# Kernel optimization log

Measured on AMD Instinct MI355X. Metric: run time of the kernel, lower is better.

The kernel has to match this reference:

```python
import jax, jax.numpy as jnp
import numpy as np
from jax import lax

DT = 0.1

def setup_inputs() -> dict:
    key = jax.random.key(0)
    ks = jax.random.split(key, 6)
    T, B, D, H, O = 4096, 16, 256, 256, 256
    x = jax.random.normal(ks[0], (T, B, D), dtype=jnp.float32)
    U_w = jax.random.normal(ks[1], (H, D), dtype=jnp.float32) / np.sqrt(D)
    U_b = jax.random.normal(ks[2], (H,), dtype=jnp.float32) * 0.1
    # underlying parameter of the ExpLambda parametrization: weight = expm(W_log)
    W_log = jax.random.normal(ks[3], (H, H), dtype=jnp.float32) * 0.01
    c_w = jax.random.normal(ks[4], (O, H), dtype=jnp.float32) / np.sqrt(H)
    c_b = jax.random.normal(ks[5], (O,), dtype=jnp.float32) * 0.1
    return {"x": x, "U_w": U_w, "U_b": U_b, "W_log": W_log, "c_w": c_w, "c_b": c_b}

def reference(x, U_w, U_b, W_log, c_w, c_b):
    # x: [T, B, D] (time-major, matching torch.transpose(x,0,1) in the original)
    T, B, D = x.shape
    H = W_log.shape[0]
    Wexp = jax.scipy.linalg.expm(W_log)          # parametrized recurrent weight
    u = jnp.einsum('tbd,hd->tbh', x, U_w) + U_b  # precompute U(x) for all steps

    def step(h, u_t):
        # h_next = h + dt * tanh(u_t - W h)
        h_next = h + DT * jnp.tanh(u_t - h @ Wexp.T)
        return h_next, h_next

    h0 = jnp.zeros((B, H), dtype=x.dtype)
    h_final, hidden = lax.scan(step, h0, u)       # hidden: [T, B, H]
    out = jnp.einsum('tbh,oh->tbo', hidden, c_w) + c_b
    # original returns h_next.unsqueeze(1) on a (1,B,H) tensor -> (1,1,B,H)
    return out, h_final[None, None]
```

## Files before the change

kernel.cpp:

```cpp
#include <hip/hip_runtime.h>
#include <math.h>

#define T_STEPS 4096
#define NB 16
#define NH 256
#define BH (NB * NH)
#define DT_STEP 0.1f

typedef __attribute__((ext_vector_type(8))) short short8;
typedef __attribute__((ext_vector_type(4))) float f32x4;

__global__ __launch_bounds__(1024) void k_init_S(const float* __restrict__ A,
                                                 float* __restrict__ S) {
    int idx = blockIdx.x * 1024 + threadIdx.x;
    int i = idx >> 8, j = idx & 255;
    S[idx] = A[idx] + (i == j ? 1.0f : 0.0f);
}

__global__ __launch_bounds__(256) void k_expm_term(const float* __restrict__ Pprev,
                                                   const float* __restrict__ A,
                                                   float* __restrict__ Pnew,
                                                   float* __restrict__ S,
                                                   float invk) {
    __shared__ float prow[256];
    int i = blockIdx.x, j = threadIdx.x;
    prow[j] = Pprev[i * 256 + j];
    __syncthreads();
    float acc = 0.f;
#pragma unroll 8
    for (int m = 0; m < 256; ++m) acc = fmaf(prow[m], A[m * 256 + j], acc);
    float v = acc * invk;
    Pnew[i * 256 + j] = v;
    S[i * 256 + j] += v;
}

__global__ __launch_bounds__(256) void k_gemm_rows(const float* __restrict__ X,
                                                   const float* __restrict__ Wm,
                                                   const float* __restrict__ bias,
                                                   float* __restrict__ Out) {
    __shared__ float4 xs4[16][64];
    const int tid = threadIdx.x;
    const long r0 = (long)blockIdx.x * 16;
    float* xs = (float*)xs4;
#pragma unroll
    for (int rr = 0; rr < 16; ++rr) xs[rr * 256 + tid] = X[(r0 + rr) * 256 + tid];
    __syncthreads();

    float acc[16];
#pragma unroll
    for (int rr = 0; rr < 16; ++rr) acc[rr] = 0.f;

    const float4* wrow = (const float4*)(Wm + tid * 256);
    for (int d4 = 0; d4 < 64; ++d4) {
        float4 w = wrow[d4];
#pragma unroll
        for (int rr = 0; rr < 16; ++rr) {
            float4 xv = xs4[rr][d4];
            acc[rr] = fmaf(w.x, xv.x, acc[rr]);
            acc[rr] = fmaf(w.y, xv.y, acc[rr]);
            acc[rr] = fmaf(w.z, xv.z, acc[rr]);
            acc[rr] = fmaf(w.w, xv.w, acc[rr]);
        }
    }
    float b = bias[tid];
#pragma unroll
    for (int rr = 0; rr < 16; ++rr) Out[(r0 + rr) * 256 + tid] = acc[rr] + b;
}

__global__ __launch_bounds__(512)
__attribute__((amdgpu_waves_per_eu(2, 2)))
void k_scan_bc6(const float* __restrict__ u,
                const float* S,
                float* hidden,
                float* __restrict__ hfin) {
    const int b   = blockIdx.x;
    const int tid = threadIdx.x;
    const int w   = tid >> 6;
    const int l   = tid & 63;
    const int lg  = l >> 4;
    const int lr  = l & 15;

    __shared__ unsigned int hlds[256];
    char* lds = (char*)hlds;

    union Frag { unsigned int u[4]; short8 v; };

    Frag ef[2][8];
#pragma unroll
    for (int j = 0; j < 2; ++j) {
        const int n = ((2 * w + j) << 4) | lr;
#pragma unroll
        for (int kt = 0; kt < 8; ++kt) {
            const int k0 = kt * 32 + lg * 8;
            const float* sp = S + (size_t)n * 256 + k0;
            float e[8];
#pragma unroll
            for (int q = 0; q < 8; ++q)
                e[q] = sp[q] - ((n == k0 + q) ? 1.0f : 0.0f);
#pragma unroll
            for (int r2 = 0; r2 < 4; ++r2) {
                unsigned int pk;
                asm volatile("v_cvt_pk_bf16_f32 %0, %1, %2"
                             : "=v"(pk) : "v"(e[2 * r2]), "v"(e[2 * r2 + 1]));
                ef[j][kt].u[r2] = pk;
            }
        }
    }

    const int j_own = (l >> 2) & 1;
    const int n_own = ((2 * w + j_own) << 4) | ((l >> 4) << 2) | (l & 3);
    const bool st = ((l & 8) == 0);
    const bool wrt = ((l & 9) == 0);

    if (tid < 256) hlds[tid] = 0u;

    const int NBLK = T_STEPS / 8;
    const size_t blkstride = 8 * (size_t)BH;

    float* hst = hidden + (size_t)b * NH + n_own;
    const float* uld = u + (size_t)b * NH + n_own + blkstride;

    float ucur[8], unxt[8], hsav[8];
    {
        const float* up0 = u + (size_t)b * NH + n_own;
#pragma unroll
        for (int q = 0; q < 8; ++q) ucur[q] = up0[q * (size_t)BH];
    }
    float hval = 0.f;
    __syncthreads();

    int roff = 0;
    for (int blk = 0; blk < NBLK; ++blk) {
#pragma unroll
        for (int s = 0; s < 8; ++s) {
            if (s == 0) {
                if (blk) {
#pragma unroll
                    for (int q = 0; q < 8; ++q)
                        if (st) hst[q * (size_t)BH] = hsav[q];
                }
#pragma unroll
                for (int q = 0; q < 8; ++q) unxt[q] = uld[q * (size_t)BH];
            }

            Frag hb[8];
#pragma unroll
            for (int kt = 0; kt < 8; ++kt)
                hb[kt].v = *(const short8*)(lds + roff + kt * 64 + lg * 16);

            f32x4 a0 = {0,0,0,0}, a1 = {0,0,0,0};
#pragma unroll
            for (int kt = 0; kt < 8; ++kt) {
                a0 = __builtin_amdgcn_mfma_f32_16x16x32_bf16(ef[0][kt].v, hb[kt].v, a0, 0, 0, 0);
                a1 = __builtin_amdgcn_mfma_f32_16x16x32_bf16(ef[1][kt].v, hb[kt].v, a1, 0, 0, 0);
            }

            f32x4 c = j_own ? a1 : a0;
            float y01 = (l & 1) ? c[1] : c[0];
            float y23 = (l & 1) ? c[3] : c[2];
            float y   = (l & 2) ? y23 : y01;

            float xa = (ucur[s] - hval) - y;
            float E2 = __expf(2.0f * xa);
            float th = fmaf(-2.0f, __builtin_amdgcn_rcpf(E2 + 1.0f), 1.0f);
            hval = fmaf(DT_STEP, th, hval);
            hsav[s] = hval;

            int nb = __builtin_amdgcn_mov_dpp(__float_as_int(hval), 0xB1, 0xF, 0xF, true);
            if (wrt) {
                unsigned int pk;
                asm volatile("v_cvt_pk_bf16_f32 %0, %1, %2"
                             : "=v"(pk) : "v"(hval), "v"(__int_as_float(nb)));
                *(unsigned int*)(lds + (roff ^ 512) + ((n_own >> 1) << 2)) = pk;
            }
            roff ^= 512;
            __syncthreads();
        }
#pragma unroll
        for (int q = 0; q < 8; ++q) ucur[q] = unxt[q];
        if (blk) hst += blkstride;
        if (blk <= NBLK - 3) uld += blkstride;
    }

#pragma unroll
    for (int q = 0; q < 8; ++q)
        if (st) hst[q * (size_t)BH] = hsav[q];
    if (st) hfin[(size_t)b * NH + n_own] = hval;
}

extern "C" void kernel_launch(void* const* d_in, const int* in_sizes, int n_in,
                              void* d_out, int out_size, void* d_ws, size_t ws_size,
                              hipStream_t stream) {
    const float* x     = (const float*)d_in[0];
    const float* U_w   = (const float*)d_in[1];
    const float* U_b   = (const float*)d_in[2];
    const float* W_log = (const float*)d_in[3];
    const float* c_w   = (const float*)d_in[4];
    const float* c_b   = (const float*)d_in[5];

    float* out    = (float*)d_out;
    float* hidden = out;
    float* hfin   = out + (long)T_STEPS * BH;

    float* ws = (float*)d_ws;
    float* S  = ws;
    float* Pa = ws + 65536;
    float* Pb = ws + 2 * 65536;
    float* u  = ws + 3 * 65536;

    k_init_S<<<64, 1024, 0, stream>>>(W_log, S);
    const float* prev = W_log;
    float* cur = Pa;
    for (int k = 2; k <= 9; ++k) {
        k_expm_term<<<256, 256, 0, stream>>>(prev, W_log, cur, S, 1.0f / (float)k);
        prev = cur;
        cur = (cur == Pa) ? Pb : Pa;
    }

    k_gemm_rows<<<4096, 256, 0, stream>>>(x, U_w, U_b, u);

    k_scan_bc6<<<NB, 512, 0, stream>>>(u, S, hidden, hfin);

    k_gemm_rows<<<4096, 256, 0, stream>>>(hidden, c_w, c_b, hidden);
}
```

Baseline: 2.211 ms.

## Replace scalar FP32 projection GEMMs with bf16 MFMA GEMMs using prepacked weights

Two new kernels replace the scalar-FMA row GEMM used for the input and output projections. A small kernel first packs each weight matrix into bf16 MFMA B-fragment layout. A second kernel then keeps each wave's A-fragments in registers and runs 16x16x32 bf16 MFMAs across all 256 output columns. This cuts the FP32 FMA cost of two 65536x256x256 GEMMs, at the price of bf16 rounding on both activations and weights. The output GEMM still runs in place on the hidden buffer.

```diff
diff --git a/kernel.cpp b/kernel.cpp
--- a/kernel.cpp
+++ b/kernel.cpp
@@ -34,37 +34,68 @@
     S[i * 256 + j] += v;
 }
 
-__global__ __launch_bounds__(256) void k_gemm_rows(const float* __restrict__ X,
-                                                   const float* __restrict__ Wm,
+__global__ __launch_bounds__(64) void k_pack_b(const float* __restrict__ W,
+                                               unsigned int* __restrict__ P) {
+    const int f = blockIdx.x;
+    const int l = threadIdx.x;
+    const int n  = ((f >> 3) << 4) | (l & 15);
+    const int k0 = ((f & 7) << 5) | ((l >> 4) << 3);
+    const float* sp = W + n * 256 + k0;
+    unsigned int o0, o1, o2, o3;
+    asm volatile("v_cvt_pk_bf16_f32 %0, %1, %2" : "=v"(o0) : "v"(sp[0]), "v"(sp[1]));
+    asm volatile("v_cvt_pk_bf16_f32 %0, %1, %2" : "=v"(o1) : "v"(sp[2]), "v"(sp[3]));
+    asm volatile("v_cvt_pk_bf16_f32 %0, %1, %2" : "=v"(o2) : "v"(sp[4]), "v"(sp[5]));
+    asm volatile("v_cvt_pk_bf16_f32 %0, %1, %2" : "=v"(o3) : "v"(sp[6]), "v"(sp[7]));
+    uint4* dst = (uint4*)(P + ((size_t)f * 64 + l) * 4);
+    *dst = make_uint4(o0, o1, o2, o3);
+}
+
+__global__ __launch_bounds__(256) void k_gemm_mfma(const float* A,
+                                                   const unsigned int* __restrict__ P,
                                                    const float* __restrict__ bias,
-                                                   float* __restrict__ Out) {
-    __shared__ float4 xs4[16][64];
+                                                   float* C) {
     const int tid = threadIdx.x;
-    const long r0 = (long)blockIdx.x * 16;
-    float* xs = (float*)xs4;
-#pragma unroll
-    for (int rr = 0; rr < 16; ++rr) xs[rr * 256 + tid] = X[(r0 + rr) * 256 + tid];
-    __syncthreads();
-
-    float acc[16];
-#pragma unroll
-    for (int rr = 0; rr < 16; ++rr) acc[rr] = 0.f;
-
-    const float4* wrow = (const float4*)(Wm + tid * 256);
-    for (int d4 = 0; d4 < 64; ++d4) {
-        float4 w = wrow[d4];
-#pragma unroll
-        for (int rr = 0; rr < 16; ++rr) {
-            float4 xv = xs4[rr][d4];
-            acc[rr] = fmaf(w.x, xv.x, acc[rr]);
-            acc[rr] = fmaf(w.y, xv.y, acc[rr]);
-            acc[rr] = fmaf(w.z, xv.z, acc[rr]);
-            acc[rr] = fmaf(w.w, xv.w, acc[rr]);
+    const int w = tid >> 6, l = tid & 63;
+    const size_t r0 = (size_t)blockIdx.x * 64 + w * 16;
+    const int arow = l & 15;
+    const int kg   = l >> 4;
+
+    union Frag { unsigned int u[4]; uint4 q; short8 v; };
+
+    Frag af[8];
+    const float* ap = A + (r0 + arow) * 256 + kg * 8;
+#pragma unroll
+    for (int kt = 0; kt < 8; ++kt) {
+        float4 x0 = *(const float4*)(ap + kt * 32);
+        float4 x1 = *(const float4*)(ap + kt * 32 + 4);
+        asm volatile("v_cvt_pk_bf16_f32 %0, %1, %2" : "=v"(af[kt].u[0]) : "v"(x0.x), "v"(x0.y));
+        asm volatile("v_cvt_pk_bf16_f32 %0, %1, %2" : "=v"(af[kt].u[1]) : "v"(x0.z), "v"(x0.w));
+        asm volatile("v_cvt_pk_bf16_f32 %0, %1, %2" : "=v"(af[kt].u[2]) : "v"(x1.x), "v"(x1.y));
+        asm volatile("v_cvt_pk_bf16_f32 %0, %1, %2" : "=v"(af[kt].u[3]) : "v"(x1.z), "v"(x1.w));
+    }
+
+    f32x4 acc[16];
+#pragma unroll
+    for (int nt = 0; nt < 16; ++nt) acc[nt] = f32x4{0.f, 0.f, 0.f, 0.f};
+
+#pragma unroll
+    for (int nt = 0; nt < 16; ++nt) {
+#pragma unroll
+        for (int kt = 0; kt < 8; ++kt) {
+            Frag bf_;
+            bf_.q = *(const uint4*)(P + (size_t)(((nt << 3) | kt) * 64 + l) * 4);
+            acc[nt] = __builtin_amdgcn_mfma_f32_16x16x32_bf16(af[kt].v, bf_.v, acc[nt], 0, 0, 0);
         }
     }
-    float b = bias[tid];
-#pragma unroll
-    for (int rr = 0; rr < 16; ++rr) Out[(r0 + rr) * 256 + tid] = acc[rr] + b;
+
+#pragma unroll
+    for (int nt = 0; nt < 16; ++nt) {
+        float b = bias[(nt << 4) | arow];
+        float* cp = C + (r0 + kg * 4) * 256 + (nt << 4) + arow;
+#pragma unroll
+        for (int r = 0; r < 4; ++r)
+            cp[(size_t)r * 256] = acc[nt][r] + b;
+    }
 }
 
 __global__ __launch_bounds__(512)
@@ -217,9 +248,14 @@
         cur = (cur == Pa) ? Pb : Pa;
     }
 
-    k_gemm_rows<<<4096, 256, 0, stream>>>(x, U_w, U_b, u);
+    unsigned int* PUw = (unsigned int*)Pa;
+    unsigned int* Pcw = (unsigned int*)Pb;
+    k_pack_b<<<128, 64, 0, stream>>>(U_w, PUw);
+    k_pack_b<<<128, 64, 0, stream>>>(c_w, Pcw);
+
+    k_gemm_mfma<<<1024, 256, 0, stream>>>(x, PUw, U_b, u);
 
     k_scan_bc6<<<NB, 512, 0, stream>>>(u, S, hidden, hfin);
 
-    k_gemm_rows<<<4096, 256, 0, stream>>>(hidden, c_w, c_b, hidden);
-}
+    k_gemm_mfma<<<1024, 256, 0, stream>>>(hidden, Pcw, c_b, hidden);
+}
```

Result: faster. 1.942 ms (-12.1%).
